# Kernel tuning notes

Measured on AMD Instinct MI355X. Metric: run time of the kernel, lower is better.

Reference implementation:

```python
import jax, jax.numpy as jnp
import numpy as np

B, N, C = 4, 4096, 1024
H, M = 16, 64          # num_heads, num_landmarks
DH = C // H
SCALE = H ** (-0.5)    # faithful to source: num_heads**-0.5
LN_EPS = 1e-5


def setup_inputs() -> dict:
    key = jax.random.key(0)
    ks = jax.random.split(key, 8)
    s = 0.02
    return {
        "x": jax.random.normal(ks[0], (B, N, C), jnp.float32),
        "ln_w": jnp.ones((C,), jnp.float32),
        "ln_b": jnp.zeros((C,), jnp.float32),
        "qkv_w": jax.random.normal(ks[1], (3 * C, C), jnp.float32) * s,
        "qkv_b": jax.random.normal(ks[2], (3 * C,), jnp.float32) * s,
        "gamma_w": jax.random.normal(ks[3], (C, C), jnp.float32) * s,
        "gamma_b": jax.random.normal(ks[4], (C,), jnp.float32) * s,
        "proj_w": jax.random.normal(ks[5], (C, C), jnp.float32) * s,
        "proj_b": jax.random.normal(ks[6], (C,), jnp.float32) * s,
    }


def _iterative_inv(K, n_iter=6):
    # Newton-Schulz pseudo-inverse on [..., M, M]
    Id = jnp.eye(K.shape[-1], dtype=K.dtype)
    KA = jnp.abs(K)
    V0 = KA.sum(axis=-2, keepdims=True).max(axis=-1, keepdims=True)
    VI = KA.sum(axis=-1, keepdims=True).max(axis=-2, keepdims=True)
    V = jnp.swapaxes(K, -2, -1) / (V0 * VI)
    for _ in range(n_iter):
        KV = K @ V
        V = 0.25 * V @ (13.0 * Id - KV @ (15.0 * Id - KV @ (7.0 * Id - KV)))
    return V


def reference(x, ln_w, ln_b, qkv_w, qkv_b, gamma_w, gamma_b, proj_w, proj_b):
    # LayerNorm
    mu = x.mean(axis=-1, keepdims=True)
    var = x.var(axis=-1, keepdims=True)
    xn = (x - mu) * jax.lax.rsqrt(var + LN_EPS) * ln_w + ln_b
    # qkv: (B,N,3C) -> (3,B,H,N,DH)
    qkv = (xn @ qkv_w.T + qkv_b).reshape(B, N, 3, H, DH).transpose(2, 0, 3, 1, 4)
    q, k, v = qkv[0], qkv[1], qkv[2]
    # landmarks: mean-pool segments of length N//M, then scale
    q_lm = q.reshape(B, H, M, N // M, DH).mean(axis=-2) * SCALE  # (B,H,M,DH)
    k_lm = k.reshape(B, H, M, N // M, DH).mean(axis=-2) * SCALE
    attn1 = jax.nn.softmax(jnp.einsum('bhnd,bhmd->bhnm', q, k_lm), axis=-1)    # (B,H,N,M)
    attn2 = jax.nn.softmax(jnp.einsum('bhmd,bhld->bhml', q_lm, k_lm), axis=-1)  # (B,H,M,M)
    attn3 = jax.nn.softmax(jnp.einsum('bhmd,bhnd->bhmn', q_lm, k), axis=-1)    # (B,H,M,N)
    attn2_inv = _iterative_inv(attn2)
    out = attn1 @ (attn2_inv @ (attn3 @ v))            # (B,H,N,DH)
    out = out.transpose(0, 2, 1, 3).reshape(B, N, C)
    out = out @ gamma_w.T + gamma_b                    # LipNorm=True branch
    out = out @ proj_w.T + proj_b                      # proj (dropout p=0 is identity)
    return out
```

## Files before the change

kernel.cpp:

```cpp
#include <hip/hip_runtime.h>
#include <stdint.h>

typedef unsigned short u16;
typedef short bf16x8 __attribute__((ext_vector_type(8)));
typedef float f32x4 __attribute__((ext_vector_type(4)));

#define MFMA16(a, b, c) __builtin_amdgcn_mfma_f32_16x16x32_bf16((a), (b), (c), 0, 0, 0)

static __device__ __forceinline__ float bfu2f(u16 u) {
  union { unsigned int i; float f; } z; z.i = ((unsigned int)u) << 16; return z.f;
}
static __device__ __forceinline__ u16 f2bfu(float f) {
  union { float f; unsigned int i; } z; z.f = f;
  unsigned int i = z.i;
  return (u16)((i + 0x7fffu + ((i >> 16) & 1u)) >> 16);
}

__device__ __forceinline__ void gload_lds16(const void* g, void* l) {
  __builtin_amdgcn_global_load_lds((const __attribute__((address_space(1))) void*)g,
                                   (__attribute__((address_space(3))) void*)l, 16, 0, 0);
}

__global__ __launch_bounds__(256) void ln_kernel(
    const float* __restrict__ x, const float* __restrict__ w,
    const float* __restrict__ b, u16* __restrict__ xn) {
  int row = blockIdx.x;
  int t = threadIdx.x;
  const float4* xr = (const float4*)(x + (size_t)row * 1024);
  float4 v = xr[t];
  float s = v.x + v.y + v.z + v.w;
  float ss = v.x * v.x + v.y * v.y + v.z * v.z + v.w * v.w;
#pragma unroll
  for (int m = 1; m < 64; m <<= 1) { s += __shfl_xor(s, m); ss += __shfl_xor(ss, m); }
  __shared__ float sb[4], ssb[4];
  int lane = t & 63, wvi = t >> 6;
  if (lane == 0) { sb[wvi] = s; ssb[wvi] = ss; }
  __syncthreads();
  s = sb[0] + sb[1] + sb[2] + sb[3];
  ss = ssb[0] + ssb[1] + ssb[2] + ssb[3];
  float mu = s * (1.0f / 1024.0f);
  float var = ss * (1.0f / 1024.0f) - mu * mu;
  float rstd = rsqrtf(var + 1e-5f);
  float4 wv4 = ((const float4*)w)[t];
  float4 bv4 = ((const float4*)b)[t];
  ushort4 o;
  o.x = f2bfu((v.x - mu) * rstd * wv4.x + bv4.x);
  o.y = f2bfu((v.y - mu) * rstd * wv4.y + bv4.y);
  o.z = f2bfu((v.z - mu) * rstd * wv4.z + bv4.z);
  o.w = f2bfu((v.w - mu) * rstd * wv4.w + bv4.w);
  ((ushort4*)xn)[(size_t)row * 256 + t] = o;
}

__global__ void cvt3_kernel(const float* __restrict__ a, u16* __restrict__ oa, int na,
                            const float* __restrict__ b, u16* __restrict__ ob, int nb,
                            const float* __restrict__ c, u16* __restrict__ oc, int nc) {
  int total = (na + nb + nc) >> 2;
  for (int i = blockIdx.x * blockDim.x + threadIdx.x; i < total; i += gridDim.x * blockDim.x) {
    int j = i << 2;
    const float* s; u16* d; int off;
    if (j < na) { s = a; d = oa; off = j; }
    else if (j < na + nb) { s = b; d = ob; off = j - na; }
    else { s = c; d = oc; off = j - na - nb; }
    float4 v = *(const float4*)(s + off);
    ushort4 o;
    o.x = f2bfu(v.x); o.y = f2bfu(v.y); o.z = f2bfu(v.z); o.w = f2bfu(v.w);
    *(ushort4*)(d + off) = o;
  }
}

template <int MODE>
__global__ __launch_bounds__(256) void gemm_bt(
    const u16* __restrict__ A, const u16* __restrict__ Bw,
    const float* __restrict__ bias,
    float* __restrict__ Cf, u16* __restrict__ Cb,
    u16* __restrict__ Qo, u16* __restrict__ Ko, u16* __restrict__ Vo,
    int M, int N, int K) {
  __shared__ __attribute__((aligned(16))) u16 As[8192];
  __shared__ __attribute__((aligned(16))) u16 Bs[8192];
  int tid = threadIdx.x;
  int lane = tid & 63;
  int w = tid >> 6;
  int wr = w >> 1, wc = w & 1;
  int r16 = lane & 15, hi = lane >> 4;
  int bx = blockIdx.x, by = blockIdx.y;

  const char* Abase = (const char*)(A + (size_t)by * 128 * K);
  const char* Bbase = (const char*)(Bw + (size_t)bx * 128 * K);
  size_t rowbytes = (size_t)K * 2;
  int l8 = lane >> 3, li = lane & 7;
  int colsw = ((li ^ l8) << 4);

  f32x4 z4 = {0.f, 0.f, 0.f, 0.f};
  f32x4 acc[4][4];
#pragma unroll
  for (int m = 0; m < 4; ++m)
#pragma unroll
    for (int n = 0; n < 4; ++n) acc[m][n] = z4;

  int nkt = K >> 6;
  for (int kt = 0; kt < nkt; ++kt) {
    int kb = kt << 7;
#pragma unroll
    for (int i = 0; i < 4; ++i) {
      int c = w * 4 + i;
      int rr = c * 8 + l8;
      gload_lds16(Abase + (size_t)rr * rowbytes + kb + colsw, (char*)As + c * 1024);
      gload_lds16(Bbase + (size_t)rr * rowbytes + kb + colsw, (char*)Bs + c * 1024);
    }
    __syncthreads();
    int sw = ((lane & 7) << 4);
#pragma unroll
    for (int kk = 0; kk < 2; ++kk) {
      int kby = (kk << 6) + (hi << 4);
      bf16x8 af[4], bfr[4];
#pragma unroll
      for (int m = 0; m < 4; ++m) {
        int row = wr * 64 + m * 16 + r16;
        af[m] = *(const bf16x8*)((const char*)As + row * 128 + (kby ^ sw));
      }
#pragma unroll
      for (int n = 0; n < 4; ++n) {
        int row = wc * 64 + n * 16 + r16;
        bfr[n] = *(const bf16x8*)((const char*)Bs + row * 128 + (kby ^ sw));
      }
#pragma unroll
      for (int m = 0; m < 4; ++m)
#pragma unroll
        for (int n = 0; n < 4; ++n) acc[m][n] = MFMA16(af[m], bfr[n], acc[m][n]);
    }
    __syncthreads();
  }

#pragma unroll
  for (int m = 0; m < 4; ++m)
#pragma unroll
    for (int n = 0; n < 4; ++n)
#pragma unroll
      for (int r = 0; r < 4; ++r) {
        int row = by * 128 + wr * 64 + m * 16 + hi * 4 + r;
        int col = bx * 128 + wc * 64 + n * 16 + r16;
        float val = acc[m][n][r] + bias[col];
        if (MODE == 0) {
          Cb[(size_t)row * N + col] = f2bfu(val);
        } else if (MODE == 1) {
          Cf[(size_t)row * N + col] = val;
        } else {
          int bb = row >> 12, nt = row & 4095;
          int jt = col >> 10, h = (col >> 6) & 15, dh = col & 63;
          u16* dst = (jt == 0) ? Qo : (jt == 1) ? Ko : Vo;
          dst[(((size_t)bb * 16 + h) * 4096 + nt) * 64 + dh] = f2bfu(val);
        }
      }
}

__global__ __launch_bounds__(64) void landmark_kernel(
    const u16* __restrict__ Q, const u16* __restrict__ K,
    float* __restrict__ qlmf, u16* __restrict__ qlmb,
    float* __restrict__ klmf, u16* __restrict__ klmb) {
  int bm = blockIdx.x;
  int bh = bm >> 6, m = bm & 63;
  int d = threadIdx.x;
  const u16* src = blockIdx.y ? K : Q;
  const u16* p = src + (((size_t)bh * 4096) + m * 64) * 64 + d;
  float s = 0.f;
#pragma unroll 8
  for (int r = 0; r < 64; ++r) s += bfu2f(p[(size_t)r * 64]);
  float val = s * (0.25f / 64.0f);
  size_t o = (size_t)bh * 4096 + m * 64 + d;
  if (blockIdx.y) { klmf[o] = val; klmb[o] = f2bfu(val); }
  else            { qlmf[o] = val; qlmb[o] = f2bfu(val); }
}

__global__ __launch_bounds__(256) void attn3_pv_kernel(
    const u16* __restrict__ qlmb, const u16* __restrict__ Kmat,
    const u16* __restrict__ Vmat, float* __restrict__ Upart,
    float* __restrict__ rspart) {
  __shared__ __attribute__((aligned(16))) u16 Elds[4][8192];
  int chunk = blockIdx.x, bh = blockIdx.y;
  int tid = threadIdx.x, lane = tid & 63, w = tid >> 6;
  int r16 = lane & 15, hi = lane >> 4;
  int keybase = chunk * 512 + w * 128;
  const u16* kb = Kmat + ((size_t)bh * 4096 + keybase) * 64;
  const u16* vb = Vmat + ((size_t)bh * 4096 + keybase) * 64;
  const u16* qb = qlmb + (size_t)bh * 4096;
  u16* eb = &Elds[w][0];
  f32x4 z4 = {0.f, 0.f, 0.f, 0.f};

  bf16x8 afr[4][2];
#pragma unroll
  for (int m = 0; m < 4; ++m)
#pragma unroll
    for (int kk = 0; kk < 2; ++kk)
      afr[m][kk] = *(const bf16x8*)(qb + (m * 16 + r16) * 64 + kk * 32 + hi * 8);

  float rs[4][4] = {};
  for (int cf = 0; cf < 8; ++cf) {
    f32x4 S[4] = {z4, z4, z4, z4};
#pragma unroll
    for (int kk = 0; kk < 2; ++kk) {
      bf16x8 bfr = *(const bf16x8*)(kb + (size_t)(cf * 16 + r16) * 64 + kk * 32 + hi * 8);
#pragma unroll
      for (int m = 0; m < 4; ++m) S[m] = MFMA16(afr[m][kk], bfr, S[m]);
    }
#pragma unroll
    for (int m = 0; m < 4; ++m)
#pragma unroll
      for (int r = 0; r < 4; ++r) {
        float e = __expf(S[m][r]);
        rs[m][r] += e;
        int row = m * 16 + hi * 4 + r;
        int key = cf * 16 + r16;
        *(u16*)((char*)eb + row * 256 + ((key * 2) ^ ((row & 7) << 4))) = f2bfu(e);
      }
  }
#pragma unroll
  for (int m = 0; m < 4; ++m)
#pragma unroll
    for (int r = 0; r < 4; ++r) {
      float v = rs[m][r];
      v += __shfl_xor(v, 1); v += __shfl_xor(v, 2);
      v += __shfl_xor(v, 4); v += __shfl_xor(v, 8);
      rs[m][r] = v;
    }
  if (r16 == 0) {
    float* rp = rspart + (((size_t)bh * 8 + chunk) * 4 + w) * 64;
#pragma unroll
    for (int m = 0; m < 4; ++m)
#pragma unroll
      for (int r = 0; r < 4; ++r) rp[m * 16 + hi * 4 + r] = rs[m][r];
  }
  __syncthreads();

  f32x4 U[4][4];
#pragma unroll
  for (int m = 0; m < 4; ++m)
#pragma unroll
    for (int df = 0; df < 4; ++df) U[m][df] = z4;
  for (int ks = 0; ks < 4; ++ks) {
    bf16x8 ea[4];
#pragma unroll
    for (int m = 0; m < 4; ++m) {
      int row = m * 16 + r16;
      ea[m] = *(const bf16x8*)((char*)eb + row * 256 + (((ks * 32 + hi * 8) * 2) ^ ((row & 7) << 4)));
    }
#pragma unroll
    for (int df = 0; df < 4; ++df) {
      bf16x8 vb8;
      const u16* vp = vb + (size_t)(ks * 32 + hi * 8) * 64 + df * 16 + r16;
#pragma unroll
      for (int j = 0; j < 8; ++j) ((short*)&vb8)[j] = (short)vp[(size_t)j * 64];
#pragma unroll
      for (int m = 0; m < 4; ++m) U[m][df] = MFMA16(ea[m], vb8, U[m][df]);
    }
  }
  float* up = Upart + (((size_t)bh * 8 + chunk) * 4 + w) * 4096;
#pragma unroll
  for (int m = 0; m < 4; ++m)
#pragma unroll
    for (int df = 0; df < 4; ++df)
#pragma unroll
      for (int r = 0; r < 4; ++r)
        up[(m * 16 + hi * 4 + r) * 64 + df * 16 + r16] = U[m][df][r];
}

__device__ __forceinline__ void mm64(const float (*AT)[68], const float (*Bm)[68],
                                     float (*C)[68], float (*CT)[68],
                                     float alpha, int tid) {
  int tr = (tid >> 4) << 2;
  int tc = (tid & 15) << 2;
  float acc[4][4] = {};
  for (int k = 0; k < 64; ++k) {
    float4 av = *(const float4*)&AT[k][tr];
    float4 bv = *(const float4*)&Bm[k][tc];
    float aa[4] = {av.x, av.y, av.z, av.w};
    float bb[4] = {bv.x, bv.y, bv.z, bv.w};
#pragma unroll
    for (int i = 0; i < 4; ++i)
#pragma unroll
      for (int j = 0; j < 4; ++j) acc[i][j] = fmaf(aa[i], bb[j], acc[i][j]);
  }
#pragma unroll
  for (int i = 0; i < 4; ++i)
#pragma unroll
    for (int j = 0; j < 4; ++j) {
      float vv = acc[i][j] * alpha;
      C[tr + i][tc + j] = vv;
      if (CT) CT[tc + j][tr + i] = vv;
    }
}

__global__ __launch_bounds__(256) void combine_ns_kernel(
    const float* __restrict__ Upart, const float* __restrict__ rspart,
    const float* __restrict__ qlmf, const float* __restrict__ klmf,
    u16* __restrict__ WT) {
  __shared__ __attribute__((aligned(16))) float A2T[64][68];
  __shared__ __attribute__((aligned(16))) float Vv[64][68];
  __shared__ __attribute__((aligned(16))) float VT[64][68];
  __shared__ __attribute__((aligned(16))) float KV[64][68];
  __shared__ __attribute__((aligned(16))) float KVT[64][68];
  __shared__ __attribute__((aligned(16))) float T2[64][68];
  __shared__ __attribute__((aligned(16))) float T4[64][68];
  __shared__ __attribute__((aligned(16))) float Tm[64][68];
  __shared__ float rsum[64], redbuf[64];
  __shared__ float v0s, scal;
  int bh = blockIdx.x, tid = threadIdx.x;

  if (tid < 64) {
    float s = 0.f;
    const float* rp = rspart + (size_t)bh * 32 * 64 + tid;
    for (int p = 0; p < 32; ++p) s += rp[p * 64];
    rsum[tid] = s;
  }
  __syncthreads();
  for (int idx = tid; idx < 4096; idx += 256) {
    float s = 0.f;
    const float* up = Upart + (size_t)bh * 32 * 4096 + idx;
    for (int p = 0; p < 32; ++p) s += up[(size_t)p * 4096];
    int r = idx >> 6, c = idx & 63;
    Tm[r][c] = s / rsum[r];
  }
  for (int idx = tid; idx < 4096; idx += 256) {
    int r = idx >> 6, c = idx & 63;
    Vv[c][r] = qlmf[(size_t)bh * 4096 + idx];
    VT[c][r] = klmf[(size_t)bh * 4096 + idx];
  }
  __syncthreads();
  mm64(&Vv[0], &VT[0], &T2[0], nullptr, 1.0f, tid);
  __syncthreads();
  if (tid < 64) {
    float mx = -1e30f;
    for (int c2 = 0; c2 < 64; ++c2) mx = fmaxf(mx, T2[tid][c2]);
    float s = 0.f;
    for (int c2 = 0; c2 < 64; ++c2) { float e = __expf(T2[tid][c2] - mx); T2[tid][c2] = e; s += e; }
    float inv = 1.f / s;
    for (int c2 = 0; c2 < 64; ++c2) { float p = T2[tid][c2] * inv; T2[tid][c2] = p; A2T[c2][tid] = p; }
  }
  __syncthreads();
  if (tid < 64) {
    float cs = 0.f;
    for (int r2 = 0; r2 < 64; ++r2) cs += fabsf(T2[r2][tid]);
    redbuf[tid] = cs;
  }
  __syncthreads();
  if (tid == 0) {
    float v0 = 0.f;
    for (int c2 = 0; c2 < 64; ++c2) v0 = fmaxf(v0, redbuf[c2]);
    v0s = v0;
  }
  __syncthreads();
  if (tid < 64) {
    float rs2 = 0.f;
    for (int c2 = 0; c2 < 64; ++c2) rs2 += fabsf(T2[tid][c2]);
    redbuf[tid] = rs2;
  }
  __syncthreads();
  if (tid == 0) {
    float vi = 0.f;
    for (int r2 = 0; r2 < 64; ++r2) vi = fmaxf(vi, redbuf[r2]);
    scal = 1.0f / (v0s * vi);
  }
  __syncthreads();
  for (int idx = tid; idx < 4096; idx += 256) {
    int r = idx >> 6, c = idx & 63;
    Vv[r][c] = A2T[r][c] * scal;
    VT[r][c] = T2[r][c] * scal;
  }
  __syncthreads();
  for (int it = 0; it < 6; ++it) {
    mm64(&A2T[0], &Vv[0], &KV[0], &KVT[0], 1.0f, tid);
    __syncthreads();
    for (int idx = tid; idx < 4096; idx += 256) {
      int r = idx >> 6, c = idx & 63;
      T2[r][c] = ((r == c) ? 7.0f : 0.0f) - KV[r][c];
    }
    __syncthreads();
    mm64(&KVT[0], &T2[0], &T4[0], nullptr, 1.0f, tid);
    __syncthreads();
    for (int idx = tid; idx < 4096; idx += 256) {
      int r = idx >> 6, c = idx & 63;
      T2[r][c] = ((r == c) ? 15.0f : 0.0f) - T4[r][c];
    }
    __syncthreads();
    mm64(&KVT[0], &T2[0], &T4[0], nullptr, 1.0f, tid);
    __syncthreads();
    for (int idx = tid; idx < 4096; idx += 256) {
      int r = idx >> 6, c = idx & 63;
      T2[r][c] = ((r == c) ? 13.0f : 0.0f) - T4[r][c];
    }
    __syncthreads();
    mm64(&VT[0], &T2[0], &T4[0], nullptr, 0.25f, tid);
    __syncthreads();
    for (int idx = tid; idx < 4096; idx += 256) {
      int r = idx >> 6, c = idx & 63;
      float vvv = T4[r][c];
      Vv[r][c] = vvv; VT[c][r] = vvv;
    }
    __syncthreads();
  }
  mm64(&VT[0], &Tm[0], &T2[0], nullptr, 1.0f, tid);
  __syncthreads();
  for (int idx = tid; idx < 4096; idx += 256) {
    int r = idx >> 6, c = idx & 63;
    WT[(size_t)bh * 4096 + c * 64 + r] = f2bfu(T2[r][c]);
  }
}

__global__ __launch_bounds__(256) void attn1_out_kernel(
    const u16* __restrict__ Q, const u16* __restrict__ klmb,
    const u16* __restrict__ WT, u16* __restrict__ AO) {
  __shared__ __attribute__((aligned(16))) u16 Elds[4][2048];
  int bh = blockIdx.y;
  int b = bh >> 4, h = bh & 15;
  int tid = threadIdx.x, lane = tid & 63, w = tid >> 6;
  int r16 = lane & 15, hi = lane >> 4;
  int rowbase = blockIdx.x * 128 + w * 32;
  const u16* qb = Q + ((size_t)bh * 4096 + rowbase) * 64;
  const u16* kb = klmb + (size_t)bh * 4096;
  const u16* wtb = WT + (size_t)bh * 4096;
  u16* eb = &Elds[w][0];
  f32x4 z4 = {0.f, 0.f, 0.f, 0.f};

  bf16x8 afr[2][2];
#pragma unroll
  for (int mi = 0; mi < 2; ++mi)
#pragma unroll
    for (int kk = 0; kk < 2; ++kk)
      afr[mi][kk] = *(const bf16x8*)(qb + (mi * 16 + r16) * 64 + kk * 32 + hi * 8);

  float rs[2][4] = {};
  for (int cf = 0; cf < 4; ++cf) {
    f32x4 S[2] = {z4, z4};
#pragma unroll
    for (int kk = 0; kk < 2; ++kk) {
      bf16x8 bfr = *(const bf16x8*)(kb + (cf * 16 + r16) * 64 + kk * 32 + hi * 8);
#pragma unroll
      for (int mi = 0; mi < 2; ++mi) S[mi] = MFMA16(afr[mi][kk], bfr, S[mi]);
    }
#pragma unroll
    for (int mi = 0; mi < 2; ++mi)
#pragma unroll
      for (int r = 0; r < 4; ++r) {
        float e = __expf(S[mi][r]);
        rs[mi][r] += e;
        int row = mi * 16 + hi * 4 + r;
        int key = cf * 16 + r16;
        *(u16*)((char*)eb + row * 128 + ((key * 2) ^ ((row & 7) << 4))) = f2bfu(e);
      }
  }
#pragma unroll
  for (int mi = 0; mi < 2; ++mi)
#pragma unroll
    for (int r = 0; r < 4; ++r) {
      float v = rs[mi][r];
      v += __shfl_xor(v, 1); v += __shfl_xor(v, 2);
      v += __shfl_xor(v, 4); v += __shfl_xor(v, 8);
      rs[mi][r] = v;
    }
  __syncthreads();

  f32x4 O[2][4];
#pragma unroll
  for (int mi = 0; mi < 2; ++mi)
#pragma unroll
    for (int df = 0; df < 4; ++df) O[mi][df] = z4;
  for (int ks = 0; ks < 2; ++ks) {
    bf16x8 ea[2];
#pragma unroll
    for (int mi = 0; mi < 2; ++mi) {
      int row = mi * 16 + r16;
      ea[mi] = *(const bf16x8*)((char*)eb + row * 128 + (((ks * 32 + hi * 8) * 2) ^ ((row & 7) << 4)));
    }
#pragma unroll
    for (int df = 0; df < 4; ++df) {
      bf16x8 wfr = *(const bf16x8*)(wtb + (df * 16 + r16) * 64 + ks * 32 + hi * 8);
#pragma unroll
      for (int mi = 0; mi < 2; ++mi) O[mi][df] = MFMA16(ea[mi], wfr, O[mi][df]);
    }
  }
#pragma unroll
  for (int mi = 0; mi < 2; ++mi)
#pragma unroll
    for (int df = 0; df < 4; ++df)
#pragma unroll
      for (int r = 0; r < 4; ++r) {
        int row = mi * 16 + hi * 4 + r;
        int n = rowbase + row;
        int col = h * 64 + df * 16 + r16;
        float val = O[mi][df][r] / rs[mi][r];
        AO[((size_t)b * 4096 + n) * 1024 + col] = f2bfu(val);
      }
}

extern "C" void kernel_launch(void* const* d_in, const int* in_sizes, int n_in,
                              void* d_out, int out_size, void* d_ws, size_t ws_size,
                              hipStream_t stream) {
  (void)in_sizes; (void)n_in; (void)out_size; (void)ws_size;
  const float* x       = (const float*)d_in[0];
  const float* ln_w    = (const float*)d_in[1];
  const float* ln_b    = (const float*)d_in[2];
  const float* qkv_w   = (const float*)d_in[3];
  const float* qkv_b   = (const float*)d_in[4];
  const float* gamma_w = (const float*)d_in[5];
  const float* gamma_b = (const float*)d_in[6];
  const float* proj_w  = (const float*)d_in[7];
  const float* proj_b  = (const float*)d_in[8];

  char* ws = (char*)d_ws;
  u16* XN     = (u16*)(ws + 0);
  u16* Qb     = (u16*)(ws + 33554432);
  u16* Kb     = (u16*)(ws + 67108864);
  u16* Vb     = (u16*)(ws + 100663296);
  u16* QKVW   = (u16*)(ws + 134217728);
  u16* GW     = (u16*)(ws + 140509184);
  u16* PW     = (u16*)(ws + 142606336);
  float* QLMF = (float*)(ws + 144703488);
  float* KLMF = (float*)(ws + 145752064);
  u16* QLMB   = (u16*)(ws + 146800640);
  u16* KLMB   = (u16*)(ws + 147324928);
  float* RSP  = (float*)(ws + 147849216);
  u16* WTb    = (u16*)(ws + 148373504);
  float* UP   = (float*)XN;

  ln_kernel<<<16384, 256, 0, stream>>>(x, ln_w, ln_b, XN);
  cvt3_kernel<<<2048, 256, 0, stream>>>(qkv_w, QKVW, 3145728,
                                        gamma_w, GW, 1048576,
                                        proj_w, PW, 1048576);
  gemm_bt<2><<<dim3(24, 128), 256, 0, stream>>>(XN, QKVW, qkv_b, nullptr, nullptr,
                                                Qb, Kb, Vb, 16384, 3072, 1024);
  landmark_kernel<<<dim3(4096, 2), 64, 0, stream>>>(Qb, Kb, QLMF, QLMB, KLMF, KLMB);
  attn3_pv_kernel<<<dim3(8, 64), 256, 0, stream>>>(QLMB, Kb, Vb, UP, RSP);
  combine_ns_kernel<<<64, 256, 0, stream>>>(UP, RSP, QLMF, KLMF, WTb);
  attn1_out_kernel<<<dim3(32, 64), 256, 0, stream>>>(Qb, KLMB, WTb, XN);
  gemm_bt<0><<<dim3(8, 128), 256, 0, stream>>>(XN, GW, gamma_b, nullptr, Kb,
                                               nullptr, nullptr, nullptr, 16384, 1024, 1024);
  gemm_bt<1><<<dim3(8, 128), 256, 0, stream>>>(Kb, PW, proj_b, (float*)d_out, nullptr,
                                               nullptr, nullptr, nullptr, 16384, 1024, 1024);
}
```

Before: 427.1 us.

## Triple-buffer GEMM LDS loads and enlarge tile to 256x128 with 8 waves

Rewrites the bf16 GEMM main loop into a three-stage software pipeline. Global-to-LDS loads for tile t+2 are issued while tile t is computed, and explicit vmcnt waits replace the full __syncthreads pair. The block grows to 512 threads covering a 256x128 output tile, so each B tile is reused across twice as many rows, and s_setprio is raised around the MFMA burst. LDS use rises to 144 KB per block, which limits occupancy, and correctness depends on the hand-tuned vmcnt counts matching the loads issued per stage.

```diff
diff --git a/kernel.cpp b/kernel.cpp
--- a/kernel.cpp
+++ b/kernel.cpp
@@ -69,26 +69,26 @@
 }
 
 template <int MODE>
-__global__ __launch_bounds__(256) void gemm_bt(
+__global__ __launch_bounds__(512, 2) void gemm_bt(
     const u16* __restrict__ A, const u16* __restrict__ Bw,
     const float* __restrict__ bias,
     float* __restrict__ Cf, u16* __restrict__ Cb,
     u16* __restrict__ Qo, u16* __restrict__ Ko, u16* __restrict__ Vo,
     int M, int N, int K) {
-  __shared__ __attribute__((aligned(16))) u16 As[8192];
-  __shared__ __attribute__((aligned(16))) u16 Bs[8192];
+  __shared__ __attribute__((aligned(16))) u16 As[3][16384];
+  __shared__ __attribute__((aligned(16))) u16 Bs[3][8192];
   int tid = threadIdx.x;
   int lane = tid & 63;
   int w = tid >> 6;
   int wr = w >> 1, wc = w & 1;
   int r16 = lane & 15, hi = lane >> 4;
+  int l8 = lane >> 3, li = lane & 7;
   int bx = blockIdx.x, by = blockIdx.y;
 
-  const char* Abase = (const char*)(A + (size_t)by * 128 * K);
+  const char* Abase = (const char*)(A + (size_t)by * 256 * K);
   const char* Bbase = (const char*)(Bw + (size_t)bx * 128 * K);
   size_t rowbytes = (size_t)K * 2;
-  int l8 = lane >> 3, li = lane & 7;
-  int colsw = ((li ^ l8) << 4);
+  int colsw = (li ^ l8) << 4;
 
   f32x4 z4 = {0.f, 0.f, 0.f, 0.f};
   f32x4 acc[4][4];
@@ -98,38 +98,80 @@
     for (int n = 0; n < 4; ++n) acc[m][n] = z4;
 
   int nkt = K >> 6;
-  for (int kt = 0; kt < nkt; ++kt) {
-    int kb = kt << 7;
-#pragma unroll
-    for (int i = 0; i < 4; ++i) {
-      int c = w * 4 + i;
-      int rr = c * 8 + l8;
-      gload_lds16(Abase + (size_t)rr * rowbytes + kb + colsw, (char*)As + c * 1024);
-      gload_lds16(Bbase + (size_t)rr * rowbytes + kb + colsw, (char*)Bs + c * 1024);
-    }
-    __syncthreads();
-    int sw = ((lane & 7) << 4);
-#pragma unroll
-    for (int kk = 0; kk < 2; ++kk) {
-      int kby = (kk << 6) + (hi << 4);
-      bf16x8 af[4], bfr[4];
-#pragma unroll
-      for (int m = 0; m < 4; ++m) {
-        int row = wr * 64 + m * 16 + r16;
-        af[m] = *(const bf16x8*)((const char*)As + row * 128 + (kby ^ sw));
-      }
-#pragma unroll
-      for (int n = 0; n < 4; ++n) {
-        int row = wc * 64 + n * 16 + r16;
-        bfr[n] = *(const bf16x8*)((const char*)Bs + row * 128 + (kby ^ sw));
-      }
+
+#define STAGE(buf, t)                                                          \
+  do {                                                                         \
+    int kb_ = (t) << 7;                                                        \
+    const char* as_ = Abase + kb_ + colsw;                                     \
+    const char* bs_ = Bbase + kb_ + colsw;                                     \
+    _Pragma("unroll")                                                          \
+    for (int i_ = 0; i_ < 4; ++i_) {                                           \
+      int r0_ = i_ * 64 + w * 8;                                               \
+      gload_lds16(as_ + (size_t)(r0_ + l8) * rowbytes,                         \
+                  (char*)As[buf] + r0_ * 128);                                 \
+    }                                                                          \
+    _Pragma("unroll")                                                          \
+    for (int i_ = 0; i_ < 2; ++i_) {                                           \
+      int r0_ = i_ * 64 + w * 8;                                               \
+      gload_lds16(bs_ + (size_t)(r0_ + l8) * rowbytes,                         \
+                  (char*)Bs[buf] + r0_ * 128);                                 \
+    }                                                                          \
+  } while (0)
+
+  STAGE(0, 0);
+  STAGE(1, 1);
+
+  int cur = 0;
+  for (int t = 0; t < nkt; ++t) {
+    int nx = cur + 2; if (nx >= 3) nx -= 3;
+    if (t + 2 < nkt) {
+      STAGE(nx, t + 2);
+      asm volatile("s_waitcnt vmcnt(12)" ::: "memory");
+    } else if (t + 1 < nkt) {
+      asm volatile("s_waitcnt vmcnt(6)" ::: "memory");
+    } else {
+      asm volatile("s_waitcnt vmcnt(0)" ::: "memory");
+    }
+    __builtin_amdgcn_s_barrier();
+    __builtin_amdgcn_sched_barrier(0);
+
+    bf16x8 af[4][2], bfr[4][2];
+#pragma unroll
+    for (int m = 0; m < 4; ++m) {
+      int row = wr * 64 + m * 16 + r16;
+      int sw = (row & 7) << 4;
+#pragma unroll
+      for (int kk = 0; kk < 2; ++kk)
+        af[m][kk] = *(const bf16x8*)((const char*)As[cur] + row * 128 +
+                                     (((kk << 6) | (hi << 4)) ^ sw));
+    }
+#pragma unroll
+    for (int n = 0; n < 4; ++n) {
+      int row = wc * 64 + n * 16 + r16;
+      int sw = (row & 7) << 4;
+#pragma unroll
+      for (int kk = 0; kk < 2; ++kk)
+        bfr[n][kk] = *(const bf16x8*)((const char*)Bs[cur] + row * 128 +
+                                      (((kk << 6) | (hi << 4)) ^ sw));
+    }
+
+    __builtin_amdgcn_s_setprio(1);
+#pragma unroll
+    for (int kk = 0; kk < 2; ++kk)
 #pragma unroll
       for (int m = 0; m < 4; ++m)
 #pragma unroll
-        for (int n = 0; n < 4; ++n) acc[m][n] = MFMA16(af[m], bfr[n], acc[m][n]);
-    }
-    __syncthreads();
-  }
+        for (int n = 0; n < 4; ++n)
+          acc[m][n] = MFMA16(af[m][kk], bfr[n][kk], acc[m][n]);
+    __builtin_amdgcn_s_setprio(0);
+
+    __builtin_amdgcn_sched_barrier(0);
+    __builtin_amdgcn_s_barrier();
+    __builtin_amdgcn_sched_barrier(0);
+
+    cur = (cur == 2) ? 0 : cur + 1;
+  }
+#undef STAGE
 
 #pragma unroll
   for (int m = 0; m < 4; ++m)
@@ -137,7 +179,7 @@
     for (int n = 0; n < 4; ++n)
 #pragma unroll
       for (int r = 0; r < 4; ++r) {
-        int row = by * 128 + wr * 64 + m * 16 + hi * 4 + r;
+        int row = by * 256 + wr * 64 + m * 16 + hi * 4 + r;
         int col = bx * 128 + wc * 64 + n * 16 + r16;
         float val = acc[m][n][r] + bias[col];
         if (MODE == 0) {
@@ -525,14 +567,14 @@
   cvt3_kernel<<<2048, 256, 0, stream>>>(qkv_w, QKVW, 3145728,
                                         gamma_w, GW, 1048576,
                                         proj_w, PW, 1048576);
-  gemm_bt<2><<<dim3(24, 128), 256, 0, stream>>>(XN, QKVW, qkv_b, nullptr, nullptr,
-                                                Qb, Kb, Vb, 16384, 3072, 1024);
+  gemm_bt<2><<<dim3(24, 64), 512, 0, stream>>>(XN, QKVW, qkv_b, nullptr, nullptr,
+                                               Qb, Kb, Vb, 16384, 3072, 1024);
   landmark_kernel<<<dim3(4096, 2), 64, 0, stream>>>(Qb, Kb, QLMF, QLMB, KLMF, KLMB);
   attn3_pv_kernel<<<dim3(8, 64), 256, 0, stream>>>(QLMB, Kb, Vb, UP, RSP);
   combine_ns_kernel<<<64, 256, 0, stream>>>(UP, RSP, QLMF, KLMF, WTb);
   attn1_out_kernel<<<dim3(32, 64), 256, 0, stream>>>(Qb, KLMB, WTb, XN);
-  gemm_bt<0><<<dim3(8, 128), 256, 0, stream>>>(XN, GW, gamma_b, nullptr, Kb,
-                                               nullptr, nullptr, nullptr, 16384, 1024, 1024);
-  gemm_bt<1><<<dim3(8, 128), 256, 0, stream>>>(Kb, PW, proj_b, (float*)d_out, nullptr,
-                                               nullptr, nullptr, nullptr, 16384, 1024, 1024);
-}
+  gemm_bt<0><<<dim3(8, 64), 512, 0, stream>>>(XN, GW, gamma_b, nullptr, Kb,
+                                              nullptr, nullptr, nullptr, 16384, 1024, 1024);
+  gemm_bt<1><<<dim3(8, 64), 512, 0, stream>>>(Kb, PW, proj_b, (float*)d_out, nullptr,
+                                              nullptr, nullptr, nullptr, 16384, 1024, 1024);
+}
```

New measurement: 446.8 us. 4.6% more time.

## Rewrite GEMM as 256x256 double-buffered pipelined kernel with 8 waves

Applied to the files above, without the earlier changes.

The shared bf16 GEMM moves from a 128x128 tile with 4 waves and a single LDS buffer to a 256x256 tile with 8 waves. Global-to-LDS loads for the next two k-steps are interleaved with MFMA phases, using manual vmcnt waits, barriers and setprio. The goal is to hide global load latency and raise arithmetic intensity per block. In exchange it uses 128KB of LDS per block, more registers, and fewer blocks (768 for QKV, 256 for the 1024-wide GEMMs), which may underfill the CUs on the smaller GEMMs.

```diff
diff --git a/kernel.cpp b/kernel.cpp
--- a/kernel.cpp
+++ b/kernel.cpp
@@ -69,76 +69,137 @@
 }
 
 template <int MODE>
-__global__ __launch_bounds__(256) void gemm_bt(
+__global__ __launch_bounds__(512, 2) void gemm_bt(
     const u16* __restrict__ A, const u16* __restrict__ Bw,
     const float* __restrict__ bias,
     float* __restrict__ Cf, u16* __restrict__ Cb,
     u16* __restrict__ Qo, u16* __restrict__ Ko, u16* __restrict__ Vo,
     int M, int N, int K) {
-  __shared__ __attribute__((aligned(16))) u16 As[8192];
-  __shared__ __attribute__((aligned(16))) u16 Bs[8192];
+  __shared__ __attribute__((aligned(16))) u16 As[2][16384];
+  __shared__ __attribute__((aligned(16))) u16 Bs[2][16384];
   int tid = threadIdx.x;
   int lane = tid & 63;
   int w = tid >> 6;
-  int wr = w >> 1, wc = w & 1;
+  int wr = w >> 2, wc = w & 3;
   int r16 = lane & 15, hi = lane >> 4;
+  int l8 = lane >> 3, li = lane & 7;
   int bx = blockIdx.x, by = blockIdx.y;
 
-  const char* Abase = (const char*)(A + (size_t)by * 128 * K);
-  const char* Bbase = (const char*)(Bw + (size_t)bx * 128 * K);
+  const char* Abase = (const char*)(A + (size_t)by * 256 * K);
+  const char* Bbase = (const char*)(Bw + (size_t)bx * 256 * K);
   size_t rowbytes = (size_t)K * 2;
-  int l8 = lane >> 3, li = lane & 7;
-  int colsw = ((li ^ l8) << 4);
+  int colsw = (li ^ l8) << 4;
+  int nkt = K >> 6;
 
   f32x4 z4 = {0.f, 0.f, 0.f, 0.f};
-  f32x4 acc[4][4];
-#pragma unroll
-  for (int m = 0; m < 4; ++m)
+  f32x4 acc[8][4];
+#pragma unroll
+  for (int m = 0; m < 8; ++m)
 #pragma unroll
     for (int n = 0; n < 4; ++n) acc[m][n] = z4;
 
-  int nkt = K >> 6;
-  for (int kt = 0; kt < nkt; ++kt) {
-    int kb = kt << 7;
-#pragma unroll
-    for (int i = 0; i < 4; ++i) {
-      int c = w * 4 + i;
-      int rr = c * 8 + l8;
-      gload_lds16(Abase + (size_t)rr * rowbytes + kb + colsw, (char*)As + c * 1024);
-      gload_lds16(Bbase + (size_t)rr * rowbytes + kb + colsw, (char*)Bs + c * 1024);
-    }
-    __syncthreads();
-    int sw = ((lane & 7) << 4);
-#pragma unroll
-    for (int kk = 0; kk < 2; ++kk) {
-      int kby = (kk << 6) + (hi << 4);
-      bf16x8 af[4], bfr[4];
-#pragma unroll
-      for (int m = 0; m < 4; ++m) {
-        int row = wr * 64 + m * 16 + r16;
-        af[m] = *(const bf16x8*)((const char*)As + row * 128 + (kby ^ sw));
-      }
-#pragma unroll
-      for (int n = 0; n < 4; ++n) {
-        int row = wc * 64 + n * 16 + r16;
-        bfr[n] = *(const bf16x8*)((const char*)Bs + row * 128 + (kby ^ sw));
-      }
-#pragma unroll
-      for (int m = 0; m < 4; ++m)
-#pragma unroll
-        for (int n = 0; n < 4; ++n) acc[m][n] = MFMA16(af[m], bfr[n], acc[m][n]);
-    }
-    __syncthreads();
-  }
-
-#pragma unroll
-  for (int m = 0; m < 4; ++m)
+#define SG_A(buf, t, r0)                                                      \
+  gload_lds16(Abase + (size_t)((r0) + w * 8 + l8) * rowbytes + ((t) << 7) +   \
+                  colsw,                                                      \
+              (char*)As[buf] + ((r0) + w * 8) * 128)
+#define SG_B(buf, t, r0)                                                      \
+  gload_lds16(Bbase + (size_t)((r0) + w * 8 + l8) * rowbytes + ((t) << 7) +   \
+                  colsw,                                                      \
+              (char*)Bs[buf] + ((r0) + w * 8) * 128)
+
+  SG_A(0, 0, 0); SG_A(0, 0, 64); SG_A(0, 0, 128); SG_A(0, 0, 192);
+  SG_B(0, 0, 0); SG_B(0, 0, 64); SG_B(0, 0, 128); SG_B(0, 0, 192);
+  SG_A(1, 1, 0); SG_A(1, 1, 128); SG_B(1, 1, 0); SG_B(1, 1, 64);
+  SG_A(1, 1, 64); SG_A(1, 1, 192);
+  asm volatile("s_waitcnt vmcnt(6)" ::: "memory");
+  __builtin_amdgcn_s_barrier();
+  __builtin_amdgcn_sched_barrier(0);
+
+  int buf = 0;
+  bf16x8 af[4][2], bfr[4][2];
+
+#define LDA(mh)                                                               \
+  _Pragma("unroll") for (int m = 0; m < 4; ++m) {                             \
+    int row = wr * 128 + (mh) * 64 + m * 16 + r16;                            \
+    int sw = (row & 7) << 4;                                                  \
+    _Pragma("unroll") for (int kk = 0; kk < 2; ++kk)                          \
+        af[m][kk] = *(const bf16x8*)(ab + row * 128 +                         \
+                                     (((kk << 6) | (hi << 4)) ^ sw));         \
+  }
+#define LDB(nh)                                                               \
+  _Pragma("unroll") for (int n = 0; n < 2; ++n) {                             \
+    int row = wc * 64 + (nh) * 32 + n * 16 + r16;                             \
+    int sw = (row & 7) << 4;                                                  \
+    _Pragma("unroll") for (int kk = 0; kk < 2; ++kk)                          \
+        bfr[(nh) * 2 + n][kk] = *(const bf16x8*)(ab2 + row * 128 +            \
+                                     (((kk << 6) | (hi << 4)) ^ sw));         \
+  }
+#define MM(mh, nh)                                                            \
+  __builtin_amdgcn_s_setprio(1);                                              \
+  _Pragma("unroll") for (int kk = 0; kk < 2; ++kk)                            \
+      _Pragma("unroll") for (int m = 0; m < 4; ++m)                           \
+          _Pragma("unroll") for (int n = 0; n < 2; ++n)                       \
+              acc[(mh) * 4 + m][(nh) * 2 + n] =                               \
+      MFMA16(af[m][kk], bfr[(nh) * 2 + n][kk], acc[(mh) * 4 + m][(nh) * 2 + n]); \
+  __builtin_amdgcn_s_setprio(0)
+
+#define BAR1                                                                  \
+  __builtin_amdgcn_s_barrier();                                               \
+  __builtin_amdgcn_sched_barrier(0)
+#define BAR2                                                                  \
+  __builtin_amdgcn_sched_barrier(0);                                          \
+  __builtin_amdgcn_s_barrier();                                               \
+  __builtin_amdgcn_sched_barrier(0)
+
+  for (int t = 0; t < nkt; ++t) {
+    const char* ab = (const char*)As[buf];
+    const char* ab2 = (const char*)Bs[buf];
+    bool s1 = (t + 1 < nkt), s2 = (t + 2 < nkt);
+    LDA(0);
+    LDB(0);
+    if (s1) { SG_B(buf ^ 1, t + 1, 128); SG_B(buf ^ 1, t + 1, 192); }
+    BAR1;
+    MM(0, 0);
+    BAR2;
+    LDB(1);
+    if (s2) { SG_A(buf, t + 2, 0); SG_A(buf, t + 2, 128); }
+    BAR1;
+    MM(0, 1);
+    BAR2;
+    LDA(1);
+    if (s2) { SG_B(buf, t + 2, 0); SG_B(buf, t + 2, 64); }
+    BAR1;
+    MM(1, 0);
+    BAR2;
+    if (s2) { SG_A(buf, t + 2, 64); SG_A(buf, t + 2, 192); }
+    BAR1;
+    MM(1, 1);
+    __builtin_amdgcn_sched_barrier(0);
+    if (s2) {
+      asm volatile("s_waitcnt vmcnt(6)" ::: "memory");
+    } else {
+      asm volatile("s_waitcnt vmcnt(0)" ::: "memory");
+    }
+    __builtin_amdgcn_s_barrier();
+    __builtin_amdgcn_sched_barrier(0);
+    buf ^= 1;
+  }
+#undef SG_A
+#undef SG_B
+#undef LDA
+#undef LDB
+#undef MM
+#undef BAR1
+#undef BAR2
+
+#pragma unroll
+  for (int m = 0; m < 8; ++m)
 #pragma unroll
     for (int n = 0; n < 4; ++n)
 #pragma unroll
       for (int r = 0; r < 4; ++r) {
-        int row = by * 128 + wr * 64 + m * 16 + hi * 4 + r;
-        int col = bx * 128 + wc * 64 + n * 16 + r16;
+        int row = by * 256 + wr * 128 + m * 16 + hi * 4 + r;
+        int col = bx * 256 + wc * 64 + n * 16 + r16;
         float val = acc[m][n][r] + bias[col];
         if (MODE == 0) {
           Cb[(size_t)row * N + col] = f2bfu(val);
@@ -525,14 +586,14 @@
   cvt3_kernel<<<2048, 256, 0, stream>>>(qkv_w, QKVW, 3145728,
                                         gamma_w, GW, 1048576,
                                         proj_w, PW, 1048576);
-  gemm_bt<2><<<dim3(24, 128), 256, 0, stream>>>(XN, QKVW, qkv_b, nullptr, nullptr,
-                                                Qb, Kb, Vb, 16384, 3072, 1024);
+  gemm_bt<2><<<dim3(12, 64), 512, 0, stream>>>(XN, QKVW, qkv_b, nullptr, nullptr,
+                                               Qb, Kb, Vb, 16384, 3072, 1024);
   landmark_kernel<<<dim3(4096, 2), 64, 0, stream>>>(Qb, Kb, QLMF, QLMB, KLMF, KLMB);
   attn3_pv_kernel<<<dim3(8, 64), 256, 0, stream>>>(QLMB, Kb, Vb, UP, RSP);
   combine_ns_kernel<<<64, 256, 0, stream>>>(UP, RSP, QLMF, KLMF, WTb);
   attn1_out_kernel<<<dim3(32, 64), 256, 0, stream>>>(Qb, KLMB, WTb, XN);
-  gemm_bt<0><<<dim3(8, 128), 256, 0, stream>>>(XN, GW, gamma_b, nullptr, Kb,
-                                               nullptr, nullptr, nullptr, 16384, 1024, 1024);
-  gemm_bt<1><<<dim3(8, 128), 256, 0, stream>>>(Kb, PW, proj_b, (float*)d_out, nullptr,
-                                               nullptr, nullptr, nullptr, 16384, 1024, 1024);
-}
+  gemm_bt<0><<<dim3(4, 64), 512, 0, stream>>>(XN, GW, gamma_b, nullptr, Kb,
+                                              nullptr, nullptr, nullptr, 16384, 1024, 1024);
+  gemm_bt<1><<<dim3(4, 64), 512, 0, stream>>>(Kb, PW, proj_b, (float*)d_out, nullptr,
+                                              nullptr, nullptr, nullptr, 16384, 1024, 1024);
+}
```

Result: faster. 378.8 us (-11.3%).
